# Performance work log

Measured on AMD Instinct MI355X. Metric: run time of the kernel, lower is better.

The kernel has to match this reference:

```python
import jax, jax.numpy as jnp
import numpy as np

IN_CH, OUT_CH, HID = 16, 16, 64
POS_DIM = 3
N_POINTS = 50000
N_EDGES = 800000
BATCH = 1

def setup_inputs() -> dict:
    key = jax.random.key(0)
    ks = jax.random.split(key, 10)
    x = jax.random.normal(ks[0], (BATCH, N_POINTS, IN_CH), dtype=jnp.float32)
    pos = jax.random.uniform(ks[1], (N_POINTS, POS_DIM), dtype=jnp.float32)
    edge_index = jax.random.randint(ks[2], (2, N_EDGES), 0, N_POINTS, dtype=jnp.int64)
    def lin(k, fan_in, fan_out):
        kw, kb = jax.random.split(k)
        bound = 1.0 / np.sqrt(fan_in)
        W = jax.random.uniform(kw, (fan_in, fan_out), minval=-bound, maxval=bound, dtype=jnp.float32)
        b = jax.random.uniform(kb, (fan_out,), minval=-bound, maxval=bound, dtype=jnp.float32)
        return W, b
    W1, b1 = lin(ks[3], 2 * POS_DIM, HID)
    Wh, bh = lin(ks[4], HID, HID)
    Wo, bo = lin(ks[5], HID, IN_CH * OUT_CH)
    return {"x": x, "pos": pos, "edge_index": edge_index,
            "W1": W1, "b1": b1, "Wh": Wh, "bh": bh, "Wo": Wo, "bo": bo}

def reference(x, pos, edge_index, W1, b1, Wh, bh, Wo, bo):
    gelu = lambda t: jax.nn.gelu(t, approximate=False)  # matches torch F.gelu default
    batch_size, n_points, in_ch = x.shape
    pos_flat = jnp.broadcast_to(pos[None], (batch_size,) + pos.shape).reshape(-1, pos.shape[-1])
    x_flat = x.reshape(-1, in_ch)
    src, dst = edge_index[0], edge_index[1]
    pos_enc = jnp.concatenate([pos_flat[src], pos_flat[dst]], axis=-1)  # [E, 2*pos_dim]
    h = gelu(pos_enc @ W1 + b1)
    h = gelu(h @ Wh + bh)
    h = h @ Wo + bo                                  # [E, in*out]
    kernel_weights = h.reshape(-1, in_ch, OUT_CH)    # [E, in, out]
    msg = jnp.einsum('eio,ei->eo', kernel_weights, x_flat[src])  # [E, out]
    out_flat = jax.ops.segment_sum(msg, dst, num_segments=batch_size * n_points)
    return out_flat.reshape(batch_size, n_points, OUT_CH)
```

## Files before the change

### kernel.cpp

```cpp
#include <hip/hip_runtime.h>

#define NPTS   50000
#define NEDGE  800000
#define NTILES 50000

typedef short bf16x8 __attribute__((ext_vector_type(8)));
typedef float f32x4  __attribute__((ext_vector_type(4)));
typedef int   i32x4  __attribute__((ext_vector_type(4)));

__device__ __forceinline__ float gelu_tanh(float v) {
    float v2 = v * v;
    float u2 = v * fmaf(v2, 0.0713548162726f, 1.5957691216057f);
    float e  = __expf(u2);
    float r  = __builtin_amdgcn_rcpf(e + 1.0f);
    return v - v * r;
}

__device__ __forceinline__ short f2bf(float f) {
    unsigned u = __builtin_bit_cast(unsigned, f);
    unsigned r = (u + 0x7FFFu + ((u >> 16) & 1u)) >> 16;
    return (short)r;
}

__device__ __forceinline__ int cvt_pk_bf16(float a, float b) {
    int r;
    asm("v_cvt_pk_bf16_f32 %0, %1, %2" : "=v"(r) : "v"(a), "v"(b));
    return r;
}

__device__ __forceinline__ int bperm(int addr, int v) {
    return __builtin_amdgcn_ds_bpermute(addr, v);
}
__device__ __forceinline__ int fbits(float v) { return __builtin_bit_cast(int, v); }
__device__ __forceinline__ float ibits(int v) { return __builtin_bit_cast(float, v); }

__global__ void zero_out_kernel(float* __restrict__ out, int n) {
    int i = blockIdx.x * blockDim.x + threadIdx.x;
    if (i < n) out[i] = 0.0f;
}

__global__ __launch_bounds__(512, 4) void edge_mfma_kernel(
    const float* __restrict__ x,
    const float* __restrict__ pos,
    const int*   __restrict__ ei,
    const float* __restrict__ W1,
    const float* __restrict__ b1,
    const float* __restrict__ Wh,
    const float* __restrict__ bh,
    const float* __restrict__ Wo,
    const float* __restrict__ bo,
    float* __restrict__ out)
{
    __shared__ bf16x8 WoF[32][64];
    __shared__ bf16x8 WhF[8][64];
    __shared__ bf16x8 W1F[4][64];
    __shared__ bf16x8 BOF[64];
    __shared__ float  bhs[64];

    const int tid = threadIdx.x;

#pragma unroll
    for (int p = 0; p < 4; ++p) {
        int e_id = p * 512 + tid;
        int s  = e_id >> 6;
        int l  = e_id & 63;
        int er_ = l & 15, g = l >> 4;
        int i  = s >> 1, kt = s & 1;
        int n  = i * 16 + er_;
        int kb = kt * 32 + g * 8;
        bf16x8 f;
#pragma unroll
        for (int j = 0; j < 8; ++j)
            f[j] = f2bf(Wo[(kb + j) * 256 + n]);
        WoF[s][l] = f;
    }
    {
        int s  = tid >> 6;
        int l  = tid & 63;
        int er_ = l & 15, g = l >> 4;
        int m  = s >> 1, kt = s & 1;
        int n  = m * 16 + er_;
        int kb = kt * 32 + g * 8;
        bf16x8 f;
#pragma unroll
        for (int j = 0; j < 8; ++j)
            f[j] = f2bf(Wh[(kb + j) * 64 + n]);
        WhF[s][l] = f;
    }
    if (tid < 256) {
        int m  = tid >> 6;
        int l  = tid & 63;
        int er_ = l & 15, g = l >> 4;
        int n  = m * 16 + er_;
        bf16x8 f;
#pragma unroll
        for (int j = 0; j < 8; ++j) {
            int k = g * 8 + j;
            float v = (k < 6) ? W1[k * 64 + n] : (k == 6 ? b1[n] : 0.0f);
            f[j] = f2bf(v);
        }
        W1F[m][l] = f;
    }
    if (tid < 64) {
        int er_ = tid & 15, g = tid >> 4;
        bf16x8 f;
#pragma unroll
        for (int j = 0; j < 8; ++j) {
            int i = g * 8 + j;
            f[j] = (g < 2) ? f2bf(bo[i * 16 + er_]) : (short)0;
        }
        BOF[tid] = f;
        bhs[tid] = bh[tid];
    }
    __syncthreads();

    const int wave = tid >> 6;
    const int lane = tid & 63;
    const int grp  = lane >> 4;
    const int er   = lane & 15;

    const int addrH0 = (er + (grp & 1) * 32) * 4;
    const int addrH1 = addrH0 + 64;
    const bool selHi = (grp >= 2);
    int addrT[4], addrD[4];
#pragma unroll
    for (int r = 0; r < 4; ++r) {
        addrT[r] = ((er >> 2) * 16 + grp * 4 + r) * 4;
        addrD[r] = (grp * 4 + r) * 4;
    }
    const int selT = er & 3;

    const bf16x8* wof = &WoF[0][lane];
    const bf16x8* whf = &WhF[0][lane];
    const bf16x8* w1f = &W1F[0][lane];
    const bf16x8  bofr = BOF[lane];
    const f32x4 zero = {0.f, 0.f, 0.f, 0.f};

    const int tbase = blockIdx.x * 32 + wave * 4;

    bf16x8 apeT[4];
    int sT[4], dT[4];
#pragma unroll
    for (int tt = 0; tt < 4; ++tt) {
        int gt = tbase + tt; if (gt >= NTILES) gt = NTILES - 1;
        int eb = gt << 4;
        int s = ei[eb + er];
        int d = ei[NEDGE + eb + er];
        s = min(max(s, 0), NPTS - 1);
        d = min(max(d, 0), NPTS - 1);
        sT[tt] = s; dT[tt] = d;
        float p0 = pos[s * 3 + 0], p1 = pos[s * 3 + 1], p2 = pos[s * 3 + 2];
        float p3 = pos[d * 3 + 0], p4 = pos[d * 3 + 1], p5 = pos[d * 3 + 2];
        const bool g0 = (grp == 0);
        bf16x8 ap;
        ap[0] = g0 ? f2bf(p0) : (short)0;
        ap[1] = g0 ? f2bf(p1) : (short)0;
        ap[2] = g0 ? f2bf(p2) : (short)0;
        ap[3] = g0 ? f2bf(p3) : (short)0;
        ap[4] = g0 ? f2bf(p4) : (short)0;
        ap[5] = g0 ? f2bf(p5) : (short)0;
        ap[6] = g0 ? (short)0x3F80 : (short)0;
        ap[7] = 0;
        apeT[tt] = ap;
    }

#pragma unroll
    for (int pp = 0; pp < 2; ++pp) {
        __syncthreads();

        const int t0 = 2 * pp;

        float xr[2][16];
#pragma unroll
        for (int q = 0; q < 2; ++q) {
            const float4* xp = reinterpret_cast<const float4*>(x + (size_t)sT[t0 + q] * 16);
            float4 a = xp[0], b = xp[1], c = xp[2], dd = xp[3];
            xr[q][0]=a.x;  xr[q][1]=a.y;  xr[q][2]=a.z;  xr[q][3]=a.w;
            xr[q][4]=b.x;  xr[q][5]=b.y;  xr[q][6]=b.z;  xr[q][7]=b.w;
            xr[q][8]=c.x;  xr[q][9]=c.y;  xr[q][10]=c.z; xr[q][11]=c.w;
            xr[q][12]=dd.x; xr[q][13]=dd.y; xr[q][14]=dd.z; xr[q][15]=dd.w;
        }

        float g1[2][4][4];
#pragma unroll
        for (int q = 0; q < 2; ++q)
#pragma unroll
            for (int m = 0; m < 4; ++m) {
                f32x4 c = __builtin_amdgcn_mfma_f32_16x16x32_bf16(w1f[m * 64], apeT[t0 + q], zero, 0, 0, 0);
#pragma unroll
                for (int r = 0; r < 4; ++r) g1[q][m][r] = gelu_tanh(c[r]);
            }

        bf16x8 B2[2][2];
#pragma unroll
        for (int q = 0; q < 2; ++q)
#pragma unroll
            for (int kt = 0; kt < 2; ++kt) {
                int pk0[2], pk1[2];
#pragma unroll
                for (int rp = 0; rp < 2; ++rp) {
                    pk0[rp] = cvt_pk_bf16(g1[q][2 * kt + 0][2 * rp], g1[q][2 * kt + 0][2 * rp + 1]);
                    pk1[rp] = cvt_pk_bf16(g1[q][2 * kt + 1][2 * rp], g1[q][2 * kt + 1][2 * rp + 1]);
                }
                i32x4 w;
#pragma unroll
                for (int h = 0; h < 2; ++h) {
                    int ah = h ? addrH1 : addrH0;
#pragma unroll
                    for (int rp = 0; rp < 2; ++rp) {
                        int vA = bperm(ah, pk0[rp]);
                        int vB = bperm(ah, pk1[rp]);
                        w[h * 2 + rp] = selHi ? vB : vA;
                    }
                }
                B2[q][kt] = __builtin_bit_cast(bf16x8, w);
            }

        float g2[2][4][4];
#pragma unroll
        for (int q = 0; q < 2; ++q)
#pragma unroll
            for (int m = 0; m < 4; ++m) {
                f32x4 c = __builtin_amdgcn_mfma_f32_16x16x32_bf16(whf[(2 * m + 0) * 64], B2[q][0], zero, 0, 0, 0);
                c = __builtin_amdgcn_mfma_f32_16x16x32_bf16(whf[(2 * m + 1) * 64], B2[q][1], c, 0, 0, 0);
                float4 b4 = *reinterpret_cast<const float4*>(&bhs[m * 16 + grp * 4]);
                float bb[4] = {b4.x, b4.y, b4.z, b4.w};
#pragma unroll
                for (int r = 0; r < 4; ++r) g2[q][m][r] = gelu_tanh(c[r] + bb[r]);
            }

        bf16x8 B3[2][2];
#pragma unroll
        for (int q = 0; q < 2; ++q)
#pragma unroll
            for (int kt = 0; kt < 2; ++kt) {
                int pk0[2], pk1[2];
#pragma unroll
                for (int rp = 0; rp < 2; ++rp) {
                    pk0[rp] = cvt_pk_bf16(g2[q][2 * kt + 0][2 * rp], g2[q][2 * kt + 0][2 * rp + 1]);
                    pk1[rp] = cvt_pk_bf16(g2[q][2 * kt + 1][2 * rp], g2[q][2 * kt + 1][2 * rp + 1]);
                }
                i32x4 w;
#pragma unroll
                for (int h = 0; h < 2; ++h) {
                    int ah = h ? addrH1 : addrH0;
#pragma unroll
                    for (int rp = 0; rp < 2; ++rp) {
                        int vA = bperm(ah, pk0[rp]);
                        int vB = bperm(ah, pk1[rp]);
                        w[h * 2 + rp] = selHi ? vB : vA;
                    }
                }
                B3[q][kt] = __builtin_bit_cast(bf16x8, w);
            }

        f32x4 msg[2];
#pragma unroll
        for (int q = 0; q < 2; ++q) {
            bf16x8 xb;
#pragma unroll
            for (int j = 0; j < 8; ++j) {
                float v = (grp == 0) ? xr[q][j] : ((grp == 1) ? xr[q][j + 8] : 0.0f);
                xb[j] = (grp < 2) ? f2bf(v) : (short)0;
            }
            msg[q] = __builtin_amdgcn_mfma_f32_16x16x32_bf16(bofr, xb, zero, 0, 0, 0);
        }

#pragma unroll
        for (int i = 0; i < 16; ++i)
#pragma unroll
            for (int q = 0; q < 2; ++q) {
                f32x4 c = __builtin_amdgcn_mfma_f32_16x16x32_bf16(wof[(2 * i + 0) * 64], B3[q][0], zero, 0, 0, 0);
                c = __builtin_amdgcn_mfma_f32_16x16x32_bf16(wof[(2 * i + 1) * 64], B3[q][1], c, 0, 0, 0);
#pragma unroll
                for (int r = 0; r < 4; ++r)
                    msg[q][r] = fmaf(xr[q][i], c[r], msg[q][r]);
            }

#pragma unroll
        for (int q = 0; q < 2; ++q) {
            const int gt = tbase + t0 + q;
            const bool ok = (gt < NTILES);
#pragma unroll
            for (int rd = 0; rd < 4; ++rd) {
                int u0 = bperm(addrT[rd], fbits(msg[q][0]));
                int u1 = bperm(addrT[rd], fbits(msg[q][1]));
                int u2 = bperm(addrT[rd], fbits(msg[q][2]));
                int u3 = bperm(addrT[rd], fbits(msg[q][3]));
                int v  = (selT == 0) ? u0 : (selT == 1) ? u1 : (selT == 2) ? u2 : u3;
                int dv = bperm(addrD[rd], dT[t0 + q]);
                if (ok) atomicAdd(out + (size_t)dv * 16 + er, ibits(v));
            }
        }
    }
}

extern "C" void kernel_launch(void* const* d_in, const int* in_sizes, int n_in,
                              void* d_out, int out_size, void* d_ws, size_t ws_size,
                              hipStream_t stream) {
    const float* x   = (const float*)d_in[0];
    const float* pos = (const float*)d_in[1];
    const int*   ei  = (const int*)d_in[2];
    const float* W1  = (const float*)d_in[3];
    const float* b1  = (const float*)d_in[4];
    const float* Wh  = (const float*)d_in[5];
    const float* bh  = (const float*)d_in[6];
    const float* Wo  = (const float*)d_in[7];
    const float* bo  = (const float*)d_in[8];
    float* out = (float*)d_out;

    zero_out_kernel<<<(out_size + 255) / 256, 256, 0, stream>>>(out, out_size);
    const int nblocks = (NTILES + 31) / 32;
    edge_mfma_kernel<<<nblocks, 512, 0, stream>>>(
        x, pos, ei, W1, b1, Wh, bh, Wo, bo, out);
}
```

Before: 201.5 us.

## Sort edges by destination and segment-reduce messages before atomic scatter

Adds a counting sort of edges by destination: histogram, three-pass scan, then a scatter of packed (src,dst) pairs into workspace. The edge kernel reads the sorted pairs and runs an in-tile segmented suffix sum via ds_bpermute, so only the head lane of each run of equal destinations issues atomics. This is meant to cut global atomic traffic and contention on the output. In exchange it adds five extra kernel launches, a pass of global atomics over all edges for the sort, and extra permute work per tile. With 16 edges per tile spread over 50000 destinations, few runs are likely to merge.

```diff
diff --git a/kernel.cpp b/kernel.cpp
--- a/kernel.cpp
+++ b/kernel.cpp
@@ -3,10 +3,17 @@
 #define NPTS   50000
 #define NEDGE  800000
 #define NTILES 50000
+#define NSCAN  49
 
 typedef short bf16x8 __attribute__((ext_vector_type(8)));
 typedef float f32x4  __attribute__((ext_vector_type(4)));
 typedef int   i32x4  __attribute__((ext_vector_type(4)));
+
+#define WS_SRCDST   0
+#define WS_COUNTS   6400000
+#define WS_CURSOR   6600000
+#define WS_PART     6800000
+#define WS_PPREF    6800256
 
 __device__ __forceinline__ float gelu_tanh(float v) {
     float v2 = v * v;
@@ -34,15 +41,85 @@
 __device__ __forceinline__ int fbits(float v) { return __builtin_bit_cast(int, v); }
 __device__ __forceinline__ float ibits(int v) { return __builtin_bit_cast(float, v); }
 
-__global__ void zero_out_kernel(float* __restrict__ out, int n) {
+
+__global__ void init_kernel(float* __restrict__ out, int* __restrict__ counts) {
     int i = blockIdx.x * blockDim.x + threadIdx.x;
-    if (i < n) out[i] = 0.0f;
-}
+    if (i < NPTS) counts[i] = 0;
+    if (i < NEDGE) out[i < 16 * NPTS ? i : 0] = 0.0f;
+}
+
+__global__ void hist_kernel(const int* __restrict__ ei, int* __restrict__ counts) {
+    int e = blockIdx.x * blockDim.x + threadIdx.x;
+    if (e >= NEDGE) return;
+    int d = ei[NEDGE + e];
+    d = min(max(d, 0), NPTS - 1);
+    atomicAdd(&counts[d], 1);
+}
+
+__global__ __launch_bounds__(1024) void scan1_kernel(const int* __restrict__ counts,
+                                                     int* __restrict__ partials) {
+    __shared__ int ws_[16];
+    int tid = threadIdx.x;
+    int i = blockIdx.x * 1024 + tid;
+    int v = (i < NPTS) ? counts[i] : 0;
+#pragma unroll
+    for (int k = 32; k >= 1; k >>= 1) v += __shfl_xor(v, k);
+    if ((tid & 63) == 0) ws_[tid >> 6] = v;
+    __syncthreads();
+    if (tid == 0) {
+        int s = 0;
+#pragma unroll
+        for (int w = 0; w < 16; ++w) s += ws_[w];
+        partials[blockIdx.x] = s;
+    }
+}
+
+__global__ void scan2_kernel(const int* __restrict__ partials, int* __restrict__ pprefix) {
+    if (threadIdx.x == 0 && blockIdx.x == 0) {
+        int run = 0;
+        for (int b = 0; b < NSCAN; ++b) { pprefix[b] = run; run += partials[b]; }
+    }
+}
+
+__global__ __launch_bounds__(1024) void scan3_kernel(const int* __restrict__ counts,
+                                                     const int* __restrict__ pprefix,
+                                                     int* __restrict__ cursor) {
+    __shared__ int buf[2][1024];
+    int tid = threadIdx.x;
+    int i = blockIdx.x * 1024 + tid;
+    int v = (i < NPTS) ? counts[i] : 0;
+    buf[0][tid] = v;
+    __syncthreads();
+    int cur = 0;
+#pragma unroll
+    for (int off = 1; off < 1024; off <<= 1) {
+        int t = buf[cur][tid] + (tid >= off ? buf[cur][tid - off] : 0);
+        buf[cur ^ 1][tid] = t;
+        cur ^= 1;
+        __syncthreads();
+    }
+    if (i < NPTS) cursor[i] = buf[cur][tid] - v + pprefix[blockIdx.x];
+}
+
+__global__ void scatter_kernel(const int* __restrict__ ei, int* __restrict__ cursor,
+                               unsigned long long* __restrict__ srcdst) {
+    int e = blockIdx.x * blockDim.x + threadIdx.x;
+    if (e >= NEDGE) return;
+    int s = ei[e];
+    int d = ei[NEDGE + e];
+    s = min(max(s, 0), NPTS - 1);
+    d = min(max(d, 0), NPTS - 1);
+    int p = atomicAdd(&cursor[d], 1);
+    unsigned long long pk = (unsigned long long)(unsigned)s |
+                            ((unsigned long long)(unsigned)d << 32);
+    __hip_atomic_store(&srcdst[p], pk, __ATOMIC_RELAXED, __HIP_MEMORY_SCOPE_AGENT);
+}
+
 
 __global__ __launch_bounds__(512, 4) void edge_mfma_kernel(
     const float* __restrict__ x,
     const float* __restrict__ pos,
-    const int*   __restrict__ ei,
+    const uint2* __restrict__ srcdst,
     const float* __restrict__ W1,
     const float* __restrict__ b1,
     const float* __restrict__ Wh,
@@ -129,6 +206,13 @@
         addrD[r] = (grp * 4 + r) * 4;
     }
     const int selT = er & 3;
+    int addrS[4];
+#pragma unroll
+    for (int k = 0; k < 4; ++k) {
+        int step = 1 << k;
+        addrS[k] = (grp * 16 + min(er + step, 15)) * 4;
+    }
+    const int addrP = (grp * 16 + max(er - 1, 0)) * 4;
 
     const bf16x8* wof = &WoF[0][lane];
     const bf16x8* whf = &WhF[0][lane];
@@ -144,10 +228,9 @@
     for (int tt = 0; tt < 4; ++tt) {
         int gt = tbase + tt; if (gt >= NTILES) gt = NTILES - 1;
         int eb = gt << 4;
-        int s = ei[eb + er];
-        int d = ei[NEDGE + eb + er];
-        s = min(max(s, 0), NPTS - 1);
-        d = min(max(d, 0), NPTS - 1);
+        uint2 sd = srcdst[eb + er];
+        int s = min((int)sd.x, NPTS - 1);
+        int d = min((int)sd.y, NPTS - 1);
         sT[tt] = s; dT[tt] = d;
         float p0 = pos[s * 3 + 0], p1 = pos[s * 3 + 1], p2 = pos[s * 3 + 2];
         float p3 = pos[d * 3 + 0], p4 = pos[d * 3 + 1], p5 = pos[d * 3 + 2];
@@ -167,7 +250,6 @@
 #pragma unroll
     for (int pp = 0; pp < 2; ++pp) {
         __syncthreads();
-
         const int t0 = 2 * pp;
 
         float xr[2][16];
@@ -281,6 +363,23 @@
         for (int q = 0; q < 2; ++q) {
             const int gt = tbase + t0 + q;
             const bool ok = (gt < NTILES);
+            const int dcur = dT[t0 + q];
+            int dn[4];
+#pragma unroll
+            for (int k = 0; k < 4; ++k) dn[k] = bperm(addrS[k], dcur);
+            const int dprev = bperm(addrP, dcur);
+            const int headf = (er == 0 || dprev != dcur) ? 1 : 0;
+#pragma unroll
+            for (int k = 0; k < 4; ++k) {
+                const int step = 1 << k;
+                const bool c = (er + step < 16) && (dn[k] == dcur);
+#pragma unroll
+                for (int r = 0; r < 4; ++r) {
+                    int o = bperm(addrS[k], fbits(msg[q][r]));
+                    msg[q][r] += c ? ibits(o) : 0.0f;
+                }
+            }
+
 #pragma unroll
             for (int rd = 0; rd < 4; ++rd) {
                 int u0 = bperm(addrT[rd], fbits(msg[q][0]));
@@ -288,8 +387,9 @@
                 int u2 = bperm(addrT[rd], fbits(msg[q][2]));
                 int u3 = bperm(addrT[rd], fbits(msg[q][3]));
                 int v  = (selT == 0) ? u0 : (selT == 1) ? u1 : (selT == 2) ? u2 : u3;
-                int dv = bperm(addrD[rd], dT[t0 + q]);
-                if (ok) atomicAdd(out + (size_t)dv * 16 + er, ibits(v));
+                int dv = bperm(addrD[rd], dcur);
+                int hf = bperm(addrD[rd], headf);
+                if (ok && hf) atomicAdd(out + (size_t)dv * 16 + er, ibits(v));
             }
         }
     }
@@ -309,8 +409,21 @@
     const float* bo  = (const float*)d_in[8];
     float* out = (float*)d_out;
 
-    zero_out_kernel<<<(out_size + 255) / 256, 256, 0, stream>>>(out, out_size);
+    char* wsb = (char*)d_ws;
+    unsigned long long* srcdst = (unsigned long long*)(wsb + WS_SRCDST);
+    int* counts  = (int*)(wsb + WS_COUNTS);
+    int* cursor  = (int*)(wsb + WS_CURSOR);
+    int* partials= (int*)(wsb + WS_PART);
+    int* pprefix = (int*)(wsb + WS_PPREF);
+
+    init_kernel<<<(NEDGE + 255) / 256, 256, 0, stream>>>(out, counts);
+    hist_kernel<<<(NEDGE + 255) / 256, 256, 0, stream>>>(ei, counts);
+    scan1_kernel<<<NSCAN, 1024, 0, stream>>>(counts, partials);
+    scan2_kernel<<<1, 64, 0, stream>>>(partials, pprefix);
+    scan3_kernel<<<NSCAN, 1024, 0, stream>>>(counts, pprefix, cursor);
+    scatter_kernel<<<(NEDGE + 255) / 256, 256, 0, stream>>>(ei, cursor, srcdst);
+
     const int nblocks = (NTILES + 31) / 32;
     edge_mfma_kernel<<<nblocks, 512, 0, stream>>>(
-        x, pos, ei, W1, b1, Wh, bh, Wo, bo, out);
-}
+        x, pos, (const uint2*)srcdst, W1, b1, Wh, bh, Wo, bo, out);
+}
```

New measurement: 283.2 us. +40.5%, slower.

## Use persistent grid-stride waves and pre-converted bf16 x features

Applied to the files above, without the earlier changes.

Replaces the one-shot grid of 1563 blocks, each doing four tiles per wave, with a fixed persistent grid of 768 blocks. Each wave now loops over tile pairs in grid-stride fashion, so the shared-memory weight fragments are loaded once per block and reused across many more edges. A new pre-pass converts x to bf16 in the workspace, which halves the gathered bytes per source node and drops the per-edge float-to-bf16 conversion. The costs are an extra kernel launch, less latency hiding because index, pos and x loads are no longer prefetched ahead across tiles, and the multiply by x now uses bf16-rounded values.

```diff
diff --git a/kernel.cpp b/kernel.cpp
--- a/kernel.cpp
+++ b/kernel.cpp
@@ -3,10 +3,14 @@
 #define NPTS   50000
 #define NEDGE  800000
 #define NTILES 50000
-
-typedef short bf16x8 __attribute__((ext_vector_type(8)));
-typedef float f32x4  __attribute__((ext_vector_type(4)));
-typedef int   i32x4  __attribute__((ext_vector_type(4)));
+#define NPAIRS 25000
+#define NBLK   768
+#define TOTW   (NBLK * 8)
+
+typedef short  bf16x8 __attribute__((ext_vector_type(8)));
+typedef float  f32x4  __attribute__((ext_vector_type(4)));
+typedef int    i32x4  __attribute__((ext_vector_type(4)));
+typedef unsigned short u16x8 __attribute__((ext_vector_type(8)));
 
 __device__ __forceinline__ float gelu_tanh(float v) {
     float v2 = v * v;
@@ -21,6 +25,9 @@
     unsigned r = (u + 0x7FFFu + ((u >> 16) & 1u)) >> 16;
     return (short)r;
 }
+__device__ __forceinline__ float bf2f(unsigned short h) {
+    return __builtin_bit_cast(float, (unsigned)h << 16);
+}
 
 __device__ __forceinline__ int cvt_pk_bf16(float a, float b) {
     int r;
@@ -39,8 +46,20 @@
     if (i < n) out[i] = 0.0f;
 }
 
+__global__ void xcopy_kernel(const float* __restrict__ x, unsigned short* __restrict__ xbf) {
+    int i = blockIdx.x * 256 + threadIdx.x;
+    if (i >= (NPTS * 16) / 4) return;
+    float4 v = reinterpret_cast<const float4*>(x)[i];
+    ushort4 o;
+    o.x = (unsigned short)f2bf(v.x);
+    o.y = (unsigned short)f2bf(v.y);
+    o.z = (unsigned short)f2bf(v.z);
+    o.w = (unsigned short)f2bf(v.w);
+    reinterpret_cast<ushort4*>(xbf)[i] = o;
+}
+
 __global__ __launch_bounds__(512, 4) void edge_mfma_kernel(
-    const float* __restrict__ x,
+    const unsigned short* __restrict__ xbf,
     const float* __restrict__ pos,
     const int*   __restrict__ ei,
     const float* __restrict__ W1,
@@ -136,49 +155,39 @@
     const bf16x8  bofr = BOF[lane];
     const f32x4 zero = {0.f, 0.f, 0.f, 0.f};
 
-    const int tbase = blockIdx.x * 32 + wave * 4;
-
-    bf16x8 apeT[4];
-    int sT[4], dT[4];
-#pragma unroll
-    for (int tt = 0; tt < 4; ++tt) {
-        int gt = tbase + tt; if (gt >= NTILES) gt = NTILES - 1;
-        int eb = gt << 4;
-        int s = ei[eb + er];
-        int d = ei[NEDGE + eb + er];
-        s = min(max(s, 0), NPTS - 1);
-        d = min(max(d, 0), NPTS - 1);
-        sT[tt] = s; dT[tt] = d;
-        float p0 = pos[s * 3 + 0], p1 = pos[s * 3 + 1], p2 = pos[s * 3 + 2];
-        float p3 = pos[d * 3 + 0], p4 = pos[d * 3 + 1], p5 = pos[d * 3 + 2];
-        const bool g0 = (grp == 0);
-        bf16x8 ap;
-        ap[0] = g0 ? f2bf(p0) : (short)0;
-        ap[1] = g0 ? f2bf(p1) : (short)0;
-        ap[2] = g0 ? f2bf(p2) : (short)0;
-        ap[3] = g0 ? f2bf(p3) : (short)0;
-        ap[4] = g0 ? f2bf(p4) : (short)0;
-        ap[5] = g0 ? f2bf(p5) : (short)0;
-        ap[6] = g0 ? (short)0x3F80 : (short)0;
-        ap[7] = 0;
-        apeT[tt] = ap;
-    }
-
-#pragma unroll
-    for (int pp = 0; pp < 2; ++pp) {
-        __syncthreads();
-
-        const int t0 = 2 * pp;
-
-        float xr[2][16];
+    const int gwave = blockIdx.x * 8 + wave;
+
+#pragma unroll 1
+    for (int pr = gwave; pr < NPAIRS; pr += TOTW) {
+        int sQ[2], dQ[2];
+        bf16x8 apeQ[2];
+        u16x8 xA[2], xB[2];
 #pragma unroll
         for (int q = 0; q < 2; ++q) {
-            const float4* xp = reinterpret_cast<const float4*>(x + (size_t)sT[t0 + q] * 16);
-            float4 a = xp[0], b = xp[1], c = xp[2], dd = xp[3];
-            xr[q][0]=a.x;  xr[q][1]=a.y;  xr[q][2]=a.z;  xr[q][3]=a.w;
-            xr[q][4]=b.x;  xr[q][5]=b.y;  xr[q][6]=b.z;  xr[q][7]=b.w;
-            xr[q][8]=c.x;  xr[q][9]=c.y;  xr[q][10]=c.z; xr[q][11]=c.w;
-            xr[q][12]=dd.x; xr[q][13]=dd.y; xr[q][14]=dd.z; xr[q][15]=dd.w;
+            const int eb = (2 * pr + q) << 4;
+            int s = ei[eb + er];
+            int d = ei[NEDGE + eb + er];
+            s = min(max(s, 0), NPTS - 1);
+            d = min(max(d, 0), NPTS - 1);
+            sQ[q] = s; dQ[q] = d;
+
+            const u16x8* xp = reinterpret_cast<const u16x8*>(xbf + (size_t)s * 16);
+            xA[q] = xp[0];
+            xB[q] = xp[1];
+
+            float p0 = pos[s * 3 + 0], p1 = pos[s * 3 + 1], p2 = pos[s * 3 + 2];
+            float p3 = pos[d * 3 + 0], p4 = pos[d * 3 + 1], p5 = pos[d * 3 + 2];
+            const bool g0 = (grp == 0);
+            bf16x8 ap;
+            ap[0] = g0 ? f2bf(p0) : (short)0;
+            ap[1] = g0 ? f2bf(p1) : (short)0;
+            ap[2] = g0 ? f2bf(p2) : (short)0;
+            ap[3] = g0 ? f2bf(p3) : (short)0;
+            ap[4] = g0 ? f2bf(p4) : (short)0;
+            ap[5] = g0 ? f2bf(p5) : (short)0;
+            ap[6] = g0 ? (short)0x3F80 : (short)0;
+            ap[7] = 0;
+            apeQ[q] = ap;
         }
 
         float g1[2][4][4];
@@ -186,7 +195,7 @@
         for (int q = 0; q < 2; ++q)
 #pragma unroll
             for (int m = 0; m < 4; ++m) {
-                f32x4 c = __builtin_amdgcn_mfma_f32_16x16x32_bf16(w1f[m * 64], apeT[t0 + q], zero, 0, 0, 0);
+                f32x4 c = __builtin_amdgcn_mfma_f32_16x16x32_bf16(w1f[m * 64], apeQ[q], zero, 0, 0, 0);
 #pragma unroll
                 for (int r = 0; r < 4; ++r) g1[q][m][r] = gelu_tanh(c[r]);
             }
@@ -260,8 +269,8 @@
             bf16x8 xb;
 #pragma unroll
             for (int j = 0; j < 8; ++j) {
-                float v = (grp == 0) ? xr[q][j] : ((grp == 1) ? xr[q][j + 8] : 0.0f);
-                xb[j] = (grp < 2) ? f2bf(v) : (short)0;
+                short v = (grp == 0) ? (short)xA[q][j] : ((grp == 1) ? (short)xB[q][j] : (short)0);
+                xb[j] = v;
             }
             msg[q] = __builtin_amdgcn_mfma_f32_16x16x32_bf16(bofr, xb, zero, 0, 0, 0);
         }
@@ -272,15 +281,14 @@
             for (int q = 0; q < 2; ++q) {
                 f32x4 c = __builtin_amdgcn_mfma_f32_16x16x32_bf16(wof[(2 * i + 0) * 64], B3[q][0], zero, 0, 0, 0);
                 c = __builtin_amdgcn_mfma_f32_16x16x32_bf16(wof[(2 * i + 1) * 64], B3[q][1], c, 0, 0, 0);
+                float xf = bf2f(i < 8 ? xA[q][i] : xB[q][i - 8]);
 #pragma unroll
                 for (int r = 0; r < 4; ++r)
-                    msg[q][r] = fmaf(xr[q][i], c[r], msg[q][r]);
+                    msg[q][r] = fmaf(xf, c[r], msg[q][r]);
             }
 
 #pragma unroll
         for (int q = 0; q < 2; ++q) {
-            const int gt = tbase + t0 + q;
-            const bool ok = (gt < NTILES);
 #pragma unroll
             for (int rd = 0; rd < 4; ++rd) {
                 int u0 = bperm(addrT[rd], fbits(msg[q][0]));
@@ -288,8 +296,8 @@
                 int u2 = bperm(addrT[rd], fbits(msg[q][2]));
                 int u3 = bperm(addrT[rd], fbits(msg[q][3]));
                 int v  = (selT == 0) ? u0 : (selT == 1) ? u1 : (selT == 2) ? u2 : u3;
-                int dv = bperm(addrD[rd], dT[t0 + q]);
-                if (ok) atomicAdd(out + (size_t)dv * 16 + er, ibits(v));
+                int dv = bperm(addrD[rd], dQ[q]);
+                atomicAdd(out + (size_t)dv * 16 + er, ibits(v));
             }
         }
     }
@@ -308,9 +316,10 @@
     const float* Wo  = (const float*)d_in[7];
     const float* bo  = (const float*)d_in[8];
     float* out = (float*)d_out;
+    unsigned short* xbf = (unsigned short*)d_ws;
 
     zero_out_kernel<<<(out_size + 255) / 256, 256, 0, stream>>>(out, out_size);
-    const int nblocks = (NTILES + 31) / 32;
-    edge_mfma_kernel<<<nblocks, 512, 0, stream>>>(
-        x, pos, ei, W1, b1, Wh, bh, Wo, bo, out);
-}
+    xcopy_kernel<<<((NPTS * 16 / 4) + 255) / 256, 256, 0, stream>>>(x, xbf);
+    edge_mfma_kernel<<<NBLK, 512, 0, stream>>>(
+        xbf, pos, ei, W1, b1, Wh, bh, Wo, bo, out);
+}
```

New measurement: 170.0 us. 1.19x faster.
